# Performance work log

Measured on AMD Instinct MI355X. Metric: run time of the kernel, lower is better.

## Reference

```python
import jax, jax.numpy as jnp
import numpy as np

NUM_HEADS = 5
TEMP = 0.3
NEG_FILL = -1e-7  # note: NOT -inf; masked entries still contribute ~exp(0) to softmax, faithful to torch code


def setup_inputs() -> dict:
    key = jax.random.key(0)
    k1, k2, k3, k4, k5 = jax.random.split(key, 5)
    B, N, F_IN, F_OUT = 8, 1024, 320, 320
    h = jax.random.normal(k1, (B, N, F_IN), dtype=jnp.float32)
    Wqk = jax.random.normal(k2, (F_IN, 2 * F_IN), dtype=jnp.float32) * (1.0 / np.sqrt(F_IN))
    bqk = jax.random.normal(k3, (2 * F_IN,), dtype=jnp.float32) * 0.01
    weight = jax.random.normal(k4, (F_IN, F_OUT), dtype=jnp.float32) * (1.0 / np.sqrt(F_OUT))
    bias = jax.random.normal(k5, (F_OUT,), dtype=jnp.float32) * 0.01
    return {"h": h, "Wqk": Wqk, "bqk": bqk, "weight": weight, "bias": bias}


def reference(h, Wqk, bqk, weight, bias):
    B, N, F = h.shape
    H = NUM_HEADS
    D = F // H
    # linear -> [b, n, 2F]; einops 'b n (h d qk)' => reshape (b, n, h, d, 2)
    qk = (h @ Wqk + bqk).reshape(B, N, H, D, 2)
    q = jnp.transpose(qk[..., 0], (0, 2, 1, 3))  # b h n d
    k = jnp.transpose(qk[..., 1], (0, 2, 1, 3))  # b h n d
    scale = D ** -0.5
    dots = jnp.einsum('bhqd,bhkd->bhqk', q, k) * scale  # b h n n
    at = dots.sum(axis=1)  # b n n  (sum over heads)
    # sort-based threshold: keep values >= descending-sorted value at index N//6
    thr = jax.lax.top_k(at, N // 6 + 1)[0][..., -1]  # b n
    adj = jnp.where(at < thr[:, :, None], jnp.asarray(NEG_FILL, at.dtype), at)
    attn = jax.nn.softmax(adj / TEMP, axis=2)  # b n n
    out_feature = jnp.einsum('bij,bjd->bid', attn, h)  # values = raw input h
    return out_feature @ weight + bias
```

## Files before the change

### kernel.cpp

```cpp
#include <hip/hip_runtime.h>
#include <hip/hip_fp16.h>


typedef __attribute__((ext_vector_type(8))) _Float16 half8;
typedef __attribute__((ext_vector_type(4))) float f32x4;

__device__ __forceinline__ void stage_tile(const __half* g, __half* lds,
                                           int nrow16, int ld, int wave, int lane) {
    const int r = lane >> 2;
    const int c = ((lane & 3) ^ ((lane >> 3) & 3)) * 8;
    for (int i = wave; i < nrow16; i += 4) {
        const __half* src = g + (long)(i * 16 + r) * ld + c;
        __builtin_amdgcn_global_load_lds(
            (const __attribute__((address_space(1))) unsigned int*)src,
            (__attribute__((address_space(3))) unsigned int*)(lds + i * 512),
            16, 0, 0);
    }
}

template <int WM, int WN, int EPI>
__global__ __launch_bounds__(256) void gemm_nt(
    const __half* __restrict__ A, const __half* __restrict__ B,
    void* __restrict__ C, void* __restrict__ C2,
    const float* __restrict__ bias,
    int K, int lda, int ldb, int ldc,
    long sA, long sB, long sC, float alpha)
{
    constexpr int BM = WM * 64;
    constexpr int BN = WN * 64;
    constexpr int BUF = BM * 32 + BN * 32;
    __shared__ __half smem[2 * BUF];

    const int tid  = threadIdx.x;
    const int lane = tid & 63;
    const int wave = tid >> 6;
    const int wm   = wave / WN;
    const int wn   = wave % WN;
    const int bz   = blockIdx.z;

    const __half* Ab = A + bz * sA + (long)blockIdx.y * BM * lda;
    const __half* Bb = B + bz * sB + (long)blockIdx.x * BN * ldb;

    f32x4 acc[4][4];
    #pragma unroll
    for (int i = 0; i < 4; ++i)
        #pragma unroll
        for (int j = 0; j < 4; ++j) acc[i][j] = (f32x4){0.f, 0.f, 0.f, 0.f};

    const int lrow = lane & 15;
    const int quad = lane >> 4;
    const int swz = (quad ^ ((lrow >> 1) & 3)) * 8;

    const int nIter = K >> 5;

    stage_tile(Ab, smem, BM / 16, lda, wave, lane);
    stage_tile(Bb, smem + BM * 32, BN / 16, ldb, wave, lane);

    for (int it = 0; it < nIter; ++it) {
        __syncthreads();
        if (it + 1 < nIter) {
            __half* nb = smem + ((it + 1) & 1) * BUF;
            const int k1 = (it + 1) << 5;
            stage_tile(Ab + k1, nb, BM / 16, lda, wave, lane);
            stage_tile(Bb + k1, nb + BM * 32, BN / 16, ldb, wave, lane);
        }
        const __half* buf = smem + (it & 1) * BUF;
        const __half* pA = buf + (wm * 64 + lrow) * 32 + swz;
        const __half* pB = buf + BM * 32 + (wn * 64 + lrow) * 32 + swz;
        half8 ah[4], bh[4];
        #pragma unroll
        for (int mt = 0; mt < 4; ++mt) ah[mt] = *(const half8*)(pA + mt * 512);
        #pragma unroll
        for (int nt = 0; nt < 4; ++nt) bh[nt] = *(const half8*)(pB + nt * 512);
        #pragma unroll
        for (int mt = 0; mt < 4; ++mt)
            #pragma unroll
            for (int nt = 0; nt < 4; ++nt)
                acc[mt][nt] = __builtin_amdgcn_mfma_f32_16x16x32_f16(
                    ah[mt], bh[nt], acc[mt][nt], 0, 0, 0);
    }

    const int row_base = blockIdx.y * BM + wm * 64;
    const int col_base = blockIdx.x * BN + wn * 64;
    #pragma unroll
    for (int mt = 0; mt < 4; ++mt)
        #pragma unroll
        for (int nt = 0; nt < 4; ++nt)
            #pragma unroll
            for (int r = 0; r < 4; ++r) {
                const int row = row_base + mt * 16 + quad * 4 + r;
                const int col = col_base + nt * 16 + lrow;
                const float v = acc[mt][nt][r];
                if (EPI == 1) {
                    const float val = v + bias[col];
                    const long idx = (long)row * 320 + (col >> 1);
                    if (col & 1) ((__half*)C2)[idx] = __float2half(val);
                    else         ((__half*)C)[idx]  = __float2half(val);
                } else if (EPI == 2) {
                    ((__half*)C)[(long)row * ldc + col] = __float2half(v);
                } else if (EPI == 3) {
                    ((float*)C)[bz * sC + (long)row * ldc + col] = v + bias[col];
                } else {
                    ((__half*)C)[bz * sC + (long)row * ldc + col] =
                        __float2half(alpha * v);
                }
            }
}

template <int EPI>
__device__ __forceinline__ void gemm_body(
    const __half* __restrict__ A, const __half* __restrict__ B,
    void* __restrict__ C, void* __restrict__ C2, const float* __restrict__ bias,
    int lda, int ldb, int ldc, int bx, int by, __half* smem)
{
    constexpr int BUF = 8192;
    const int tid  = threadIdx.x;
    const int lane = tid & 63;
    const int wave = tid >> 6;
    const int wm   = wave >> 1;
    const int wn   = wave & 1;

    const __half* Ab = A + (long)by * 128 * lda;
    const __half* Bb = B + (long)bx * 128 * ldb;

    f32x4 acc[4][4];
    #pragma unroll
    for (int i = 0; i < 4; ++i)
        #pragma unroll
        for (int j = 0; j < 4; ++j) acc[i][j] = (f32x4){0.f, 0.f, 0.f, 0.f};

    const int lrow = lane & 15;
    const int quad = lane >> 4;
    const int swz = (quad ^ ((lrow >> 1) & 3)) * 8;

    stage_tile(Ab, smem, 8, lda, wave, lane);
    stage_tile(Bb, smem + 4096, 8, ldb, wave, lane);

    for (int it = 0; it < 10; ++it) {
        __syncthreads();
        if (it + 1 < 10) {
            __half* nb = smem + ((it + 1) & 1) * BUF;
            stage_tile(Ab + (it + 1) * 32, nb, 8, lda, wave, lane);
            stage_tile(Bb + (it + 1) * 32, nb + 4096, 8, ldb, wave, lane);
        }
        const __half* buf = smem + (it & 1) * BUF;
        const __half* pA = buf + (wm * 64 + lrow) * 32 + swz;
        const __half* pB = buf + 4096 + (wn * 64 + lrow) * 32 + swz;
        half8 ah[4], bh[4];
        #pragma unroll
        for (int mt = 0; mt < 4; ++mt) ah[mt] = *(const half8*)(pA + mt * 512);
        #pragma unroll
        for (int nt = 0; nt < 4; ++nt) bh[nt] = *(const half8*)(pB + nt * 512);
        #pragma unroll
        for (int mt = 0; mt < 4; ++mt)
            #pragma unroll
            for (int nt = 0; nt < 4; ++nt)
                acc[mt][nt] = __builtin_amdgcn_mfma_f32_16x16x32_f16(
                    ah[mt], bh[nt], acc[mt][nt], 0, 0, 0);
    }

    const int row_base = by * 128 + wm * 64;
    const int col_base = bx * 128 + wn * 64;
    #pragma unroll
    for (int mt = 0; mt < 4; ++mt)
        #pragma unroll
        for (int nt = 0; nt < 4; ++nt)
            #pragma unroll
            for (int r = 0; r < 4; ++r) {
                const int row = row_base + mt * 16 + quad * 4 + r;
                const int col = col_base + nt * 16 + lrow;
                const float v = acc[mt][nt][r];
                if (EPI == 1) {
                    const float val = v + bias[col];
                    const long idx = (long)row * 320 + (col >> 1);
                    if (col & 1) ((__half*)C2)[idx] = __float2half(val);
                    else         ((__half*)C)[idx]  = __float2half(val);
                } else {
                    ((__half*)C)[(long)row * ldc + col] = __float2half(v);
                }
            }
}

__global__ __launch_bounds__(256) void g1_combined(
    const __half* __restrict__ h16, const __half* __restrict__ wTp,
    const __half* __restrict__ WqkT, __half* __restrict__ hWT,
    __half* __restrict__ Q, __half* __restrict__ Kb,
    const float* __restrict__ bqk)
{
    __shared__ __half smem[2 * 8192];
    const int bx = blockIdx.x;
    if (bx < 192) {
        gemm_body<2>(wTp, h16, hWT, nullptr, nullptr,
                     320, 320, 8192, bx % 64, bx / 64, smem);
    } else {
        const int b = bx - 192;
        gemm_body<1>(h16, WqkT, Q, Kb, bqk,
                     320, 320, 320, b % 5, b / 5, smem);
    }
}

__global__ __launch_bounds__(256) void prep_all(
    const float* __restrict__ h, ushort4* __restrict__ h16,
    const float* __restrict__ Wqk, __half* __restrict__ WqkT,
    const float* __restrict__ weight, __half* __restrict__ wTp)
{
    const int bx = blockIdx.x;
    if (bx < 2560) {
        const int i = bx * 256 + threadIdx.x;
        const float4 v = ((const float4*)h)[i];
        ushort4 o;
        o.x = __half_as_ushort(__float2half(v.x));
        o.y = __half_as_ushort(__float2half(v.y));
        o.z = __half_as_ushort(__float2half(v.z));
        o.w = __half_as_ushort(__float2half(v.w));
        h16[i] = o;
        return;
    }
    __shared__ float t[32][33];
    const float* src;
    __half* dst;
    int ldS, ldT, c0, r0;
    if (bx < 2760) {
        const int b = bx - 2560;
        src = Wqk; dst = WqkT; ldS = 640; ldT = 320;
        c0 = (b % 20) * 32; r0 = (b / 20) * 32;
    } else {
        const int b = bx - 2760;
        src = weight; dst = wTp; ldS = 320; ldT = 320;
        c0 = (b % 10) * 32; r0 = (b / 10) * 32;
    }
    const int lx = threadIdx.x & 31, ly = threadIdx.x >> 5;
    #pragma unroll
    for (int i = 0; i < 4; ++i)
        t[ly + 8 * i][lx] = src[(long)(r0 + ly + 8 * i) * ldS + c0 + lx];
    __syncthreads();
    #pragma unroll
    for (int i = 0; i < 4; ++i)
        dst[(long)(c0 + ly + 8 * i) * ldT + r0 + lx] = __float2half(t[lx][ly + 8 * i]);
}

__global__ __launch_bounds__(256) void topk_softmax(const __half* __restrict__ at,
                                                    __half* __restrict__ attn)
{
    __shared__ int hist[4][256];
    const int lane = threadIdx.x & 63;
    const int wave = threadIdx.x >> 6;
    const long row = (long)blockIdx.x * 4 + wave;

    unsigned short vs[16];
    {
        const uint4* p = (const uint4*)(at + row * 1024 + lane * 16);
        *(uint4*)&vs[0] = p[0];
        *(uint4*)&vs[8] = p[1];
    }

    unsigned key[16];
    #pragma unroll
    for (int i = 0; i < 16; ++i) {
        const unsigned u = vs[i];
        key[i] = (u & 0x8000u) ? ((~u) & 0xFFFFu) : (u | 0x8000u);
    }

    unsigned prefix = 0, pmask = 0;
    int kk = 171;

    #pragma unroll
    for (int pass = 0; pass < 2; ++pass) {
        const int shift = 8 - 8 * pass;
        *(int4*)&hist[wave][lane * 4] = make_int4(0, 0, 0, 0);
        __syncthreads();
        #pragma unroll
        for (int i = 0; i < 16; ++i) {
            if ((key[i] & pmask) == prefix)
                atomicAdd(&hist[wave][(key[i] >> shift) & 255], 1);
        }
        __syncthreads();
        const int4 hh = *(const int4*)&hist[wave][lane * 4];
        const int s = hh.x + hh.y + hh.z + hh.w;
        int suf = s;
        #pragma unroll
        for (int off = 1; off < 64; off <<= 1) {
            const int o = __shfl_down(suf, off);
            if (lane + off < 64) suf += o;
        }
        const int cgt3 = suf - s;
        const int cgt2 = cgt3 + hh.w;
        const int cgt1 = cgt2 + hh.z;
        const int cgt0 = cgt1 + hh.y;
        int pick = 0x7FFFFFFF;
        if (cgt3 < kk && kk <= cgt3 + hh.w) pick = ((4 * lane + 3) << 16) | (kk - cgt3);
        if (cgt2 < kk && kk <= cgt2 + hh.z) pick = ((4 * lane + 2) << 16) | (kk - cgt2);
        if (cgt1 < kk && kk <= cgt1 + hh.y) pick = ((4 * lane + 1) << 16) | (kk - cgt1);
        if (cgt0 < kk && kk <= cgt0 + hh.x) pick = ((4 * lane + 0) << 16) | (kk - cgt0);
        #pragma unroll
        for (int off = 32; off > 0; off >>= 1) pick = min(pick, __shfl_xor(pick, off));
        const unsigned digit = (unsigned)(pick >> 16);
        kk = pick & 0xFFFF;
        prefix |= digit << shift;
        pmask  |= 0xFFu << shift;
        if (pass == 0) __syncthreads();
    }

    const unsigned short tu = (prefix & 0x8000u) ? (unsigned short)(prefix & 0x7FFFu)
                                                 : (unsigned short)((~prefix) & 0xFFFFu);
    const float thr = __half2float(__ushort_as_half(tu));

    float lg[16];
    float mx = -3.4e38f;
    #pragma unroll
    for (int i = 0; i < 16; ++i) {
        const float v = __half2float(__ushort_as_half(vs[i]));
        const float a = (v < thr) ? -1e-7f : v;
        lg[i] = a * (1.0f / 0.3f);
        mx = fmaxf(mx, lg[i]);
    }
    #pragma unroll
    for (int off = 32; off > 0; off >>= 1) mx = fmaxf(mx, __shfl_xor(mx, off));

    float e[16];
    float sum = 0.f;
    #pragma unroll
    for (int i = 0; i < 16; ++i) { e[i] = __expf(lg[i] - mx); sum += e[i]; }
    #pragma unroll
    for (int off = 32; off > 0; off >>= 1) sum += __shfl_xor(sum, off);
    const float inv = 1.0f / sum;

    unsigned short os[16];
    #pragma unroll
    for (int i = 0; i < 16; ++i) os[i] = __half_as_ushort(__float2half(e[i] * inv));
    uint4* q = (uint4*)(attn + row * 1024 + lane * 16);
    q[0] = *(const uint4*)&os[0];
    q[1] = *(const uint4*)&os[8];
}

extern "C" void kernel_launch(void* const* d_in, const int* in_sizes, int n_in,
                              void* d_out, int out_size, void* d_ws, size_t ws_size,
                              hipStream_t stream) {
    (void)in_sizes; (void)n_in; (void)out_size; (void)ws_size;

    const float* h      = (const float*)d_in[0];
    const float* Wqk    = (const float*)d_in[1];
    const float* bqk    = (const float*)d_in[2];
    const float* weight = (const float*)d_in[3];
    const float* bias   = (const float*)d_in[4];
    float* out = (float*)d_out;

    char* p = (char*)d_ws;
    __half* at   = (__half*)p; p += 8388608L * 2;
    __half* attn = (__half*)p; p += 8388608L * 2;
    __half* h16  = (__half*)p; p += 2621440L * 2;
    __half* Q    = (__half*)p; p += 2621440L * 2;
    __half* Kb   = (__half*)p; p += 2621440L * 2;
    __half* WqkT = (__half*)p; p += 640L * 320 * 2;
    __half* wTp  = (__half*)p; p += 384L * 320 * 2;
    __half* hWT  = (__half*)p; p += 384L * 8192 * 2;

    prep_all<<<2860, 256, 0, stream>>>(h, (ushort4*)h16, Wqk, WqkT, weight, wTp);

    g1_combined<<<512, 256, 0, stream>>>(h16, wTp, WqkT, hWT, Q, Kb, bqk);

    gemm_nt<2, 2, 4><<<dim3(8, 8, 8), 256, 0, stream>>>(
        Q, Kb, at, nullptr, nullptr,
        320, 320, 320, 1024, 327680, 327680, 1048576, 0.125f);

    topk_softmax<<<2048, 256, 0, stream>>>(at, attn);

    gemm_nt<4, 1, 3><<<dim3(5, 4, 8), 256, 0, stream>>>(
        attn, hWT, out, nullptr, bias,
        1024, 1024, 8192, 320, 1048576, 1024, 327680, 1.0f);
}
```

Baseline: 138.4 us.

## Split-K the final attn·hW GEMM four ways with atomic accumulation

The last GEMM (attn × hWT) ran on only 160 blocks of 256-row tiles over K=1024. This change splits K into four slices, raising the grid to 640 blocks, and each block atomically adds its partial sums into the fp32 output. The output is pre-filled with the bias by extra blocks added to the prep kernel. It trades better CU occupancy on a 256-CU device for atomic traffic on the output and nondeterministic summation order.

```diff
diff --git a/kernel.cpp b/kernel.cpp
--- a/kernel.cpp
+++ b/kernel.cpp
@@ -38,8 +38,18 @@
     const int wn   = wave % WN;
     const int bz   = blockIdx.z;
 
-    const __half* Ab = A + bz * sA + (long)blockIdx.y * BM * lda;
-    const __half* Bb = B + bz * sB + (long)blockIdx.x * BN * ldb;
+    int by = blockIdx.y;
+    int ks = 0;
+    int nIter = K >> 5;
+    if (EPI == 5) {
+        ks = by & 3;
+        by >>= 2;
+        nIter = K >> 7;
+    }
+    const int kOff = (EPI == 5) ? ks * (K >> 2) : 0;
+
+    const __half* Ab = A + bz * sA + (long)by * BM * lda + kOff;
+    const __half* Bb = B + bz * sB + (long)blockIdx.x * BN * ldb + kOff;
 
     f32x4 acc[4][4];
     #pragma unroll
@@ -50,8 +60,6 @@
     const int lrow = lane & 15;
     const int quad = lane >> 4;
     const int swz = (quad ^ ((lrow >> 1) & 3)) * 8;
-
-    const int nIter = K >> 5;
 
     stage_tile(Ab, smem, BM / 16, lda, wave, lane);
     stage_tile(Bb, smem + BM * 32, BN / 16, ldb, wave, lane);
@@ -80,7 +88,7 @@
                     ah[mt], bh[nt], acc[mt][nt], 0, 0, 0);
     }
 
-    const int row_base = blockIdx.y * BM + wm * 64;
+    const int row_base = by * BM + wm * 64;
     const int col_base = blockIdx.x * BN + wn * 64;
     #pragma unroll
     for (int mt = 0; mt < 4; ++mt)
@@ -98,11 +106,11 @@
                     else         ((__half*)C)[idx]  = __float2half(val);
                 } else if (EPI == 2) {
                     ((__half*)C)[(long)row * ldc + col] = __float2half(v);
-                } else if (EPI == 3) {
-                    ((float*)C)[bz * sC + (long)row * ldc + col] = v + bias[col];
-                } else {
+                } else if (EPI == 4) {
                     ((__half*)C)[bz * sC + (long)row * ldc + col] =
                         __float2half(alpha * v);
+                } else {
+                    atomicAdd(&((float*)C)[bz * sC + (long)row * ldc + col], v);
                 }
             }
 }
@@ -202,7 +210,8 @@
 __global__ __launch_bounds__(256) void prep_all(
     const float* __restrict__ h, ushort4* __restrict__ h16,
     const float* __restrict__ Wqk, __half* __restrict__ WqkT,
-    const float* __restrict__ weight, __half* __restrict__ wTp)
+    const float* __restrict__ weight, __half* __restrict__ wTp,
+    const float* __restrict__ bias, float4* __restrict__ out4)
 {
     const int bx = blockIdx.x;
     if (bx < 2560) {
@@ -214,6 +223,11 @@
         o.z = __half_as_ushort(__float2half(v.z));
         o.w = __half_as_ushort(__float2half(v.w));
         h16[i] = o;
+        return;
+    }
+    if (bx >= 2860) {
+        const int i = (bx - 2860) * 256 + threadIdx.x;
+        out4[i] = ((const float4*)bias)[i % 80];
         return;
     }
     __shared__ float t[32][33];
@@ -355,7 +369,8 @@
     __half* wTp  = (__half*)p; p += 384L * 320 * 2;
     __half* hWT  = (__half*)p; p += 384L * 8192 * 2;
 
-    prep_all<<<2860, 256, 0, stream>>>(h, (ushort4*)h16, Wqk, WqkT, weight, wTp);
+    prep_all<<<5420, 256, 0, stream>>>(h, (ushort4*)h16, Wqk, WqkT, weight, wTp,
+                                       bias, (float4*)out);
 
     g1_combined<<<512, 256, 0, stream>>>(h16, wTp, WqkT, hWT, Q, Kb, bqk);
 
@@ -365,7 +380,7 @@
 
     topk_softmax<<<2048, 256, 0, stream>>>(at, attn);
 
-    gemm_nt<4, 1, 3><<<dim3(5, 4, 8), 256, 0, stream>>>(
-        attn, hWT, out, nullptr, bias,
+    gemm_nt<4, 1, 5><<<dim3(5, 16, 8), 256, 0, stream>>>(
+        attn, hWT, out, nullptr, nullptr,
         1024, 1024, 8192, 320, 1048576, 1024, 327680, 1.0f);
 }
```

Measured after the change: 160.1 us. 1.16x slower.
